# Kernel optimization log

Hardware: AMD Instinct MI355X
Metric: run time of the kernel (lower is better)

The kernel has to match this reference:

```python
import jax, jax.numpy as jnp
import numpy as np

B, S, D = 2, 2048, 4096
H, G, HD = 32, 8, 128          # num_heads, num_kv_groups, head_dim
GROUP = H // G                  # group_size = 4
SCALE = HD ** -0.5


def setup_inputs() -> dict:
    key = jax.random.key(0)
    ks = jax.random.split(key, 6)
    x = jax.random.normal(ks[0], (B, S, D), dtype=jnp.float32)
    # Linear weights stored as [in, out] (y = x @ W), no bias, 0.02 init scale
    Wq = jax.random.normal(ks[1], (D, H * HD), dtype=jnp.float32) * 0.02
    Wk = jax.random.normal(ks[2], (D, G * HD), dtype=jnp.float32) * 0.02
    Wv = jax.random.normal(ks[3], (D, G * HD), dtype=jnp.float32) * 0.02
    Wo = jax.random.normal(ks[4], (H * HD, D), dtype=jnp.float32) * 0.02
    # RoPE tables: [S, HD], duplicated-half layout (rotate-half convention)
    inv_freq = 1.0 / (10000.0 ** (jnp.arange(0, HD, 2, dtype=jnp.float32) / HD))
    angles = jnp.arange(S, dtype=jnp.float32)[:, None] * inv_freq[None, :]  # [S, HD/2]
    angles = jnp.concatenate([angles, angles], axis=-1)                      # [S, HD]
    cos = jnp.cos(angles)
    sin = jnp.sin(angles)
    # causal mask: True = masked (strict upper triangle)
    mask = jnp.triu(jnp.ones((S, S), dtype=bool), k=1)
    return {"x": x, "Wq": Wq, "Wk": Wk, "Wv": Wv, "Wo": Wo,
            "cos": cos, "sin": sin, "mask": mask, "start_pos": 0}


def _rope(t, cos, sin, offset):
    # t: [B, h, S, HD]; cos/sin: [S_total, HD]
    n = t.shape[2]
    c = jax.lax.dynamic_slice_in_dim(cos, offset, n, axis=0)  # [n, HD]
    s = jax.lax.dynamic_slice_in_dim(sin, offset, n, axis=0)
    t1, t2 = t[..., : HD // 2], t[..., HD // 2:]
    rotated = jnp.concatenate([-t2, t1], axis=-1)
    return t * c[None, None] + rotated * s[None, None]


def reference(x, Wq, Wk, Wv, Wo, cos, sin, mask, start_pos):
    # projections
    q = (x @ Wq).reshape(B, S, H, HD).transpose(0, 2, 1, 3)   # [B,H,S,HD]
    k = (x @ Wk).reshape(B, S, G, HD).transpose(0, 2, 1, 3)   # [B,G,S,HD]
    v = (x @ Wv).reshape(B, S, G, HD).transpose(0, 2, 1, 3)   # [B,G,S,HD]
    # RoPE (no cache: prev_len = 0)
    q = _rope(q, cos, sin, start_pos) * SCALE
    k = _rope(k, cos, sin, start_pos)
    # GQA: expand kv groups to full heads (repeat_interleave along head dim)
    k_r = jnp.repeat(k, GROUP, axis=1)                         # [B,H,S,HD]
    v_r = jnp.repeat(v, GROUP, axis=1)
    scores = jnp.einsum('bhqd,bhkd->bhqk', q, k_r)             # [B,H,S,S]
    scores = jnp.where(mask[None, None], -jnp.inf, scores)
    w = jax.nn.softmax(scores, axis=-1)
    ctx = jnp.einsum('bhqk,bhkd->bhqd', w, v_r)                # [B,H,S,HD]
    ctx = ctx.transpose(0, 2, 1, 3).reshape(B, S, H * HD)
    out = ctx @ Wo                                             # [B,S,D]
    return out
```

## Files before the change

### kernel.cpp

```cpp
#include <hip/hip_runtime.h>
#include <hip/hip_bf16.h>
#include <math.h>

#define B_ 2
#define S_ 2048
#define D_ 4096
#define H_ 32
#define G_ 8
#define HD_ 128
#define GROUP_ 4
#define SCALE_ 0.08838834764831845f

typedef short bfv8 __attribute__((ext_vector_type(8)));
typedef float f32x4 __attribute__((ext_vector_type(4)));

__device__ __forceinline__ f32x4 mfma16(bfv8 a, bfv8 b, f32x4 c) {
  return __builtin_amdgcn_mfma_f32_16x16x32_bf16(a, b, c, 0, 0, 0);
}

__device__ __forceinline__ ushort f2bf_bits(float f) {
  __hip_bfloat16 h = __float2bfloat16(f);
  return *reinterpret_cast<ushort*>(&h);
}

__device__ __forceinline__ void gload16(const short* g, short* l) {
  __builtin_amdgcn_global_load_lds(
      (const __attribute__((address_space(1))) void*)g,
      (__attribute__((address_space(3))) void*)l, 16, 0, 0);
}

__global__ __launch_bounds__(256) void k_cvt(const float* __restrict__ in,
                                             ushort* __restrict__ out, int n4) {
  int i = blockIdx.x * 256 + threadIdx.x;
  if (i >= n4) return;
  float4 v = *(const float4*)(in + (size_t)i * 4);
  ushort4 o;
  o.x = f2bf_bits(v.x); o.y = f2bf_bits(v.y); o.z = f2bf_bits(v.z); o.w = f2bf_bits(v.w);
  *(ushort4*)(out + (size_t)i * 4) = o;
}

__global__ __launch_bounds__(256) void k_transpose(const float* __restrict__ in,
                                                   ushort* __restrict__ out,
                                                   int R, int C) {
  __shared__ ushort tile[32][33];
  int bc = blockIdx.x * 32;
  int br = blockIdx.y * 32;
  int tx = threadIdx.x;
  int ty = threadIdx.y;
  for (int ii = 0; ii < 4; ii++) {
    int i = ty + ii * 8;
    tile[i][tx] = f2bf_bits(in[(size_t)(br + i) * C + bc + tx]);
  }
  __syncthreads();
  for (int ii = 0; ii < 4; ii++) {
    int i = ty + ii * 8;
    out[(size_t)(bc + i) * R + br + tx] = tile[tx][i];
  }
}

__global__ __launch_bounds__(256) void k_transpose_v(const ushort* __restrict__ v,
                                                     ushort* __restrict__ vt) {
  __shared__ ushort tile[32][33];
  int bg = blockIdx.z;
  int b = bg / G_, g = bg % G_;
  int s0 = blockIdx.y * 32;
  int h0 = blockIdx.x * 32;
  int tx = threadIdx.x, ty = threadIdx.y;
  const ushort* src = v + (size_t)b * S_ * G_ * HD_ + (size_t)g * HD_;
  ushort* dst = vt + (size_t)(b * G_ + g) * HD_ * S_;
  for (int ii = 0; ii < 4; ii++) {
    int i = ty + ii * 8;
    tile[i][tx] = src[(size_t)(s0 + i) * (G_ * HD_) + h0 + tx];
  }
  __syncthreads();
  for (int ii = 0; ii < 4; ii++) {
    int i = ty + ii * 8;
    dst[(size_t)(h0 + i) * S_ + s0 + tx] = tile[tx][i];
  }
}

__global__ __launch_bounds__(64) void k_rope(__hip_bfloat16* __restrict__ t,
                                             const float* __restrict__ cosb,
                                             const float* __restrict__ sinb,
                                             int nheads, float scale) {
  int blk = blockIdx.x;
  int head = blk % nheads;
  int row = blk / nheads;
  int s = row & (S_ - 1);
  int l = threadIdx.x;
  size_t base = (size_t)row * nheads * HD_ + (size_t)head * HD_;
  float x1 = __bfloat162float(t[base + l]);
  float x2 = __bfloat162float(t[base + 64 + l]);
  float c1 = cosb[s * HD_ + l];
  float sn1 = sinb[s * HD_ + l];
  float c2 = cosb[s * HD_ + 64 + l];
  float sn2 = sinb[s * HD_ + 64 + l];
  t[base + l] = __float2bfloat16((x1 * c1 - x2 * sn1) * scale);
  t[base + 64 + l] = __float2bfloat16((x2 * c2 + x1 * sn2) * scale);
}

template <typename OT>
__global__ __launch_bounds__(256) void k_gemm_bt(const __hip_bfloat16* __restrict__ Ab,
                                                 const __hip_bfloat16* __restrict__ BTb,
                                                 OT* __restrict__ Cb,
                                                 int M, int N, int K) {
  __shared__ short sA[128 * 32];
  __shared__ short sB[128 * 32];
  int t = threadIdx.x;
  int w = t >> 6;
  int l = t & 63;
  int row0 = blockIdx.y * 128;
  int col0 = blockIdx.x * 128;
  int wr = (w >> 1) * 64;
  int wc = (w & 1) * 64;
  int fr = l & 15;
  int fq = l >> 4;
  int fo = fq * 8;
  int srow = l >> 2;
  int schk = (l & 3) * 8;

  const short* gA = (const short*)Ab;
  const short* gB = (const short*)BTb;

  f32x4 acc[4][4];
#pragma unroll
  for (int m = 0; m < 4; m++)
#pragma unroll
    for (int n = 0; n < 4; n++) acc[m][n] = (f32x4){0.f, 0.f, 0.f, 0.f};

  for (int k0 = 0; k0 < K; k0 += 32) {
    __syncthreads();
#pragma unroll
    for (int j = 0; j < 2; j++) {
      int r = w * 32 + j * 16;
      gload16(gA + (size_t)(row0 + r + srow) * K + k0 + schk, &sA[r * 32]);
      gload16(gB + (size_t)(col0 + r + srow) * K + k0 + schk, &sB[r * 32]);
    }
    __syncthreads();
    bfv8 af[4], bff[4];
#pragma unroll
    for (int m = 0; m < 4; m++) af[m] = *(const bfv8*)(sA + (wr + m * 16 + fr) * 32 + fo);
#pragma unroll
    for (int n = 0; n < 4; n++) bff[n] = *(const bfv8*)(sB + (wc + n * 16 + fr) * 32 + fo);
#pragma unroll
    for (int m = 0; m < 4; m++)
#pragma unroll
      for (int n = 0; n < 4; n++)
        acc[m][n] = mfma16(af[m], bff[n], acc[m][n]);
  }
#pragma unroll
  for (int m = 0; m < 4; m++)
#pragma unroll
    for (int n = 0; n < 4; n++)
#pragma unroll
      for (int j = 0; j < 4; j++) {
        int r = row0 + wr + m * 16 + fq * 4 + j;
        int c = col0 + wc + n * 16 + fr;
        if constexpr (__is_same(OT, float)) {
          Cb[(size_t)r * N + c] = acc[m][n][j];
        } else {
          Cb[(size_t)r * N + c] = __float2bfloat16(acc[m][n][j]);
        }
      }
}

template <typename OT>
__global__ __launch_bounds__(512, 2) void k_gemm256(const __hip_bfloat16* __restrict__ Ab,
                                                    const __hip_bfloat16* __restrict__ BTb,
                                                    OT* __restrict__ Cb,
                                                    int M, int N, int K) {
  __shared__ short sA[2][2][8192];
  __shared__ short sB[2][2][8192];
  int tid = threadIdx.x;
  int wid = tid >> 6;
  int l = tid & 63;
  int wr = (wid >> 2) * 128;
  int wc = (wid & 3) * 64;
  int fr = l & 15, fq = l >> 4;
  int cswz = (fq ^ ((fr >> 1) & 3)) * 8;
  int row0 = blockIdx.y * 256, col0 = blockIdx.x * 256;
  int sr = l >> 2;
  int schunk = ((l & 3) ^ (((wid * 16 + sr) >> 1) & 3)) * 8;
  const short* gA = (const short*)Ab;
  const short* gB = (const short*)BTb;

  f32x4 acc[8][4];
#pragma unroll
  for (int m = 0; m < 8; m++)
#pragma unroll
    for (int n = 0; n < 4; n++) acc[m][n] = (f32x4){0.f, 0.f, 0.f, 0.f};

#define STAGE256(buf, kh, isB, kt)                                                   \
  {                                                                                  \
    const short* g_ = (isB) ? gB : gA;                                               \
    int b0_ = (isB) ? col0 : row0;                                                   \
    short* s_ = (isB) ? &sB[buf][kh][0] : &sA[buf][kh][0];                           \
    int k0_ = (kt) * 64 + (kh) * 32;                                                 \
    _Pragma("unroll")                                                                \
    for (int i_ = 0; i_ < 2; i_++) {                                                 \
      int r_ = i_ * 128 + wid * 16 + sr;                                             \
      gload16(g_ + (size_t)(b0_ + r_) * K + k0_ + schunk,                            \
              s_ + (i_ * 128 + wid * 16) * 32);                                      \
    }                                                                                \
  }

  bfv8 bf[4];
#define COMPUTE256(cur, kh, mg, loadB)                                               \
  {                                                                                  \
    if (loadB) {                                                                     \
      _Pragma("unroll")                                                              \
      for (int n_ = 0; n_ < 4; n_++)                                                 \
        bf[n_] = *(const bfv8*)&sB[cur][kh][(wc + n_ * 16 + fr) * 32 + cswz];        \
    }                                                                                \
    bfv8 af_[4];                                                                     \
    _Pragma("unroll")                                                                \
    for (int j_ = 0; j_ < 4; j_++)                                                   \
      af_[j_] = *(const bfv8*)&sA[cur][kh][(wr + ((mg) * 4 + j_) * 16 + fr) * 32 + cswz]; \
    __builtin_amdgcn_s_setprio(1);                                                   \
    _Pragma("unroll")                                                                \
    for (int j_ = 0; j_ < 4; j_++)                                                   \
      _Pragma("unroll")                                                              \
      for (int n_ = 0; n_ < 4; n_++)                                                 \
        acc[(mg) * 4 + j_][n_] = mfma16(af_[j_], bf[n_], acc[(mg) * 4 + j_][n_]);    \
    __builtin_amdgcn_s_setprio(0);                                                   \
  }

  int NT = K / 64;
  STAGE256(0, 0, false, 0);
  STAGE256(0, 0, true, 0);
  STAGE256(0, 1, false, 0);
  STAGE256(0, 1, true, 0);

  for (int t = 0; t < NT - 1; t++) {
    int cur = t & 1, nxt = cur ^ 1;
    asm volatile("s_waitcnt vmcnt(4)" ::: "memory");
    __builtin_amdgcn_s_barrier();
    STAGE256(nxt, 0, false, t + 1);
    COMPUTE256(cur, 0, 0, true);
    STAGE256(nxt, 0, true, t + 1);
    COMPUTE256(cur, 0, 1, false);
    asm volatile("s_waitcnt vmcnt(4)" ::: "memory");
    __builtin_amdgcn_s_barrier();
    STAGE256(nxt, 1, false, t + 1);
    COMPUTE256(cur, 1, 0, true);
    STAGE256(nxt, 1, true, t + 1);
    COMPUTE256(cur, 1, 1, false);
  }
  {
    int cur = (NT - 1) & 1;
    asm volatile("s_waitcnt vmcnt(4)" ::: "memory");
    __builtin_amdgcn_s_barrier();
    COMPUTE256(cur, 0, 0, true);
    COMPUTE256(cur, 0, 1, false);
    asm volatile("s_waitcnt vmcnt(0)" ::: "memory");
    __builtin_amdgcn_s_barrier();
    COMPUTE256(cur, 1, 0, true);
    COMPUTE256(cur, 1, 1, false);
  }
#undef STAGE256
#undef COMPUTE256

#pragma unroll
  for (int m = 0; m < 8; m++)
#pragma unroll
    for (int n = 0; n < 4; n++)
#pragma unroll
      for (int j = 0; j < 4; j++) {
        int r = row0 + wr + m * 16 + fq * 4 + j;
        int c = col0 + wc + n * 16 + fr;
        if constexpr (__is_same(OT, float)) {
          Cb[(size_t)r * N + c] = acc[m][n][j];
        } else {
          Cb[(size_t)r * N + c] = __float2bfloat16(acc[m][n][j]);
        }
      }
}

#define PSTR 68
__global__ __launch_bounds__(512) void k_attn2(const __hip_bfloat16* __restrict__ Qb,
                                               const __hip_bfloat16* __restrict__ Kb,
                                               const __hip_bfloat16* __restrict__ VTb,
                                               __hip_bfloat16* __restrict__ ctx) {
  __shared__ short sK[64 * 128];
  __shared__ short sV[128 * 64];
  __shared__ short sP[8][16 * PSTR];

  const int nQB = S_ / 128;
  int blk = blockIdx.x;
  int qb = (nQB - 1) - (blk % nQB);
  int bh = blk / nQB;
  int h = bh % H_;
  int b = bh / H_;
  int g = h / GROUP_;
  int q0 = qb * 128;

  int t = threadIdx.x;
  int wid = t >> 6;
  int l = t & 63;
  int fr = l & 15, fq = l >> 4, fo = fq * 8;
  int wq0 = q0 + wid * 16;

  const short* qp = (const short*)Qb + (size_t)b * S_ * H_ * HD_ + (size_t)h * HD_;
  const short* kp = (const short*)Kb + (size_t)b * S_ * G_ * HD_ + (size_t)g * HD_;
  const short* vp = (const short*)VTb + (size_t)(b * G_ + g) * HD_ * S_;

  bfv8 qf[4];
#pragma unroll
  for (int c = 0; c < 4; c++)
    qf[c] = *(const bfv8*)(qp + (size_t)(wq0 + fr) * (H_ * HD_) + c * 32 + fo);

  f32x4 acc[8];
#pragma unroll
  for (int n = 0; n < 8; n++) acc[n] = (f32x4){0.f, 0.f, 0.f, 0.f};
  float m[4], ll[4];
#pragma unroll
  for (int j = 0; j < 4; j++) { m[j] = -INFINITY; ll[j] = 0.f; }

  int krow_i = l >> 4;
  int kchk = l & 15;
  int vrow_i = l >> 3;
  int vchk = l & 7;

  int nkt = 2 * qb + 2;
  for (int kt = 0; kt < nkt; kt++) {
    int k0 = kt * 64;
#pragma unroll
    for (int j = 0; j < 2; j++) {
      int base = wid * 8 + j * 4;
      int r = base + krow_i;
      gload16(kp + (size_t)(k0 + r) * (G_ * HD_) + ((kchk ^ (r & 7)) * 8), &sK[base * 128]);
    }
#pragma unroll
    for (int j = 0; j < 2; j++) {
      int base = wid * 16 + j * 8;
      int r = base + vrow_i;
      gload16(vp + (size_t)r * S_ + k0 + ((vchk ^ (r & 7)) * 8), &sV[base * 64]);
    }
    __syncthreads();

    f32x4 sf[4];
#pragma unroll
    for (int ks = 0; ks < 4; ks++) {
      sf[ks] = (f32x4){0.f, 0.f, 0.f, 0.f};
      int row = ks * 16 + fr;
      int rx = row & 7;
#pragma unroll
      for (int c = 0; c < 4; c++) {
        bfv8 kf = *(const bfv8*)&sK[row * 128 + (((c * 4 + fq) ^ rx) * 8)];
        sf[ks] = mfma16(qf[c], kf, sf[ks]);
      }
    }

    float p[4][4], sc[4], red[4];
#pragma unroll
    for (int j = 0; j < 4; j++) {
      int q = wq0 + fq * 4 + j;
#pragma unroll
      for (int ks = 0; ks < 4; ks++)
        if (k0 + ks * 16 + fr > q) sf[ks][j] = -INFINITY;
      red[j] = fmaxf(fmaxf(sf[0][j], sf[1][j]), fmaxf(sf[2][j], sf[3][j]));
    }
#pragma unroll
    for (int off = 1; off < 16; off <<= 1)
#pragma unroll
      for (int j = 0; j < 4; j++)
        red[j] = fmaxf(red[j], __shfl_xor(red[j], off, 64));
#pragma unroll
    for (int j = 0; j < 4; j++) {
      float nm = fmaxf(m[j], red[j]);
      sc[j] = __expf(m[j] - nm);
      m[j] = nm;
#pragma unroll
      for (int ks = 0; ks < 4; ks++) p[ks][j] = __expf(sf[ks][j] - nm);
      red[j] = (p[0][j] + p[1][j]) + (p[2][j] + p[3][j]);
    }
#pragma unroll
    for (int off = 1; off < 16; off <<= 1)
#pragma unroll
      for (int j = 0; j < 4; j++)
        red[j] += __shfl_xor(red[j], off, 64);
#pragma unroll
    for (int j = 0; j < 4; j++) {
      ll[j] = ll[j] * sc[j] + red[j];
#pragma unroll
      for (int n = 0; n < 8; n++) acc[n][j] *= sc[j];
#pragma unroll
      for (int ks = 0; ks < 4; ks++)
        sP[wid][(fq * 4 + j) * PSTR + ks * 16 + fr] = f2bf_bits(p[ks][j]);
    }

    bfv8 pa0 = *(const bfv8*)&sP[wid][fr * PSTR + fo];
    bfv8 pa1 = *(const bfv8*)&sP[wid][fr * PSTR + 32 + fo];
#pragma unroll
    for (int n = 0; n < 8; n++) {
      int row = n * 16 + fr;
      int rx = row & 7;
      bfv8 vf0 = *(const bfv8*)&sV[row * 64 + ((fq ^ rx) * 8)];
      bfv8 vf1 = *(const bfv8*)&sV[row * 64 + (((4 + fq) ^ rx) * 8)];
      acc[n] = mfma16(pa0, vf0, acc[n]);
      acc[n] = mfma16(pa1, vf1, acc[n]);
    }
    __syncthreads();
  }

#pragma unroll
  for (int n = 0; n < 8; n++)
#pragma unroll
    for (int j = 0; j < 4; j++) {
      int q = wq0 + fq * 4 + j;
      float o = acc[n][j] / ll[j];
      ctx[(size_t)(b * S_ + q) * (H_ * HD_) + h * HD_ + n * 16 + fr] = __float2bfloat16(o);
    }
}

extern "C" void kernel_launch(void* const* d_in, const int* in_sizes, int n_in,
                              void* d_out, int out_size, void* d_ws, size_t ws_size,
                              hipStream_t stream) {
  (void)in_sizes; (void)n_in; (void)out_size; (void)ws_size;
  const float* x    = (const float*)d_in[0];
  const float* Wq   = (const float*)d_in[1];
  const float* Wk   = (const float*)d_in[2];
  const float* Wv   = (const float*)d_in[3];
  const float* Wo   = (const float*)d_in[4];
  const float* cosb = (const float*)d_in[5];
  const float* sinb = (const float*)d_in[6];

  char* ws = (char*)d_ws;
  __hip_bfloat16* xb  = (__hip_bfloat16*)(ws + 0);
  __hip_bfloat16* WqT = (__hip_bfloat16*)(ws + 33554432);
  __hip_bfloat16* WkT = (__hip_bfloat16*)(ws + 67108864);
  __hip_bfloat16* WvT = (__hip_bfloat16*)(ws + 75497472);
  __hip_bfloat16* Qb  = (__hip_bfloat16*)(ws + 83886080);
  __hip_bfloat16* Kb  = (__hip_bfloat16*)(ws + 117440512);
  __hip_bfloat16* Vb  = (__hip_bfloat16*)(ws + 125829120);
  __hip_bfloat16* VTb = (__hip_bfloat16*)(ws + 134217728);
  __hip_bfloat16* Cx  = xb;

  dim3 tb(32, 8);
  k_cvt<<<(B_ * S_ * D_ / 4 + 255) / 256, 256, 0, stream>>>(x, (ushort*)xb, B_ * S_ * D_ / 4);
  k_transpose<<<dim3(128, 128), tb, 0, stream>>>(Wq, (ushort*)WqT, 4096, 4096);
  k_transpose<<<dim3(32, 128), tb, 0, stream>>>(Wk, (ushort*)WkT, 4096, 1024);
  k_transpose<<<dim3(32, 128), tb, 0, stream>>>(Wv, (ushort*)WvT, 4096, 1024);

  k_gemm256<__hip_bfloat16><<<dim3(16, 16), 512, 0, stream>>>(xb, WqT, Qb, 4096, 4096, 4096);
  k_gemm_bt<__hip_bfloat16><<<dim3(8, 32), 256, 0, stream>>>(xb, WkT, Kb, 4096, 1024, 4096);
  k_gemm_bt<__hip_bfloat16><<<dim3(8, 32), 256, 0, stream>>>(xb, WvT, Vb, 4096, 1024, 4096);

  k_transpose<<<dim3(128, 128), tb, 0, stream>>>(Wo, (ushort*)WqT, 4096, 4096);

  k_rope<<<4096 * 32, 64, 0, stream>>>(Qb, cosb, sinb, 32, SCALE_);
  k_rope<<<4096 * 8, 64, 0, stream>>>(Kb, cosb, sinb, 8, 1.0f);

  k_transpose_v<<<dim3(4, 64, 16), tb, 0, stream>>>((const ushort*)Vb, (ushort*)VTb);

  k_attn2<<<B_ * H_ * (S_ / 128), 512, 0, stream>>>(Qb, Kb, VTb, Cx);

  k_gemm256<float><<<dim3(16, 16), 512, 0, stream>>>(Cx, WqT, (float*)d_out, 4096, 4096, 4096);
}
```

Measured before the change: 829.5 us.

## Fuse K/V projection GEMMs, vectorize weight transpose, batch RoPE heads per block

Merges the K and V projections into one GEMM by treating the adjacent WkT/WvT buffers as a single 2048-wide weight, writing an interleaved KV buffer that attention and the V transpose read with a doubled stride. The fp32-to-bf16 weight transpose now uses float4 loads and ushort4 stores with a 1D block. RoPE processes four heads per 256-thread block instead of one head per 64-thread block. These aim to cut launch count and improve memory efficiency in the small pre-processing kernels, at the cost of relying on the workspace adjacency of the K and V weights.

```diff
diff --git a/kernel.cpp b/kernel.cpp
--- a/kernel.cpp
+++ b/kernel.cpp
@@ -9,6 +9,7 @@
 #define G_ 8
 #define HD_ 128
 #define GROUP_ 4
+#define KVSTR_ (2 * G_ * HD_)
 #define SCALE_ 0.08838834764831845f
 
 typedef short bfv8 __attribute__((ext_vector_type(8)));
@@ -42,35 +43,42 @@
 __global__ __launch_bounds__(256) void k_transpose(const float* __restrict__ in,
                                                    ushort* __restrict__ out,
                                                    int R, int C) {
-  __shared__ ushort tile[32][33];
+  __shared__ ushort tile[32][36];
   int bc = blockIdx.x * 32;
   int br = blockIdx.y * 32;
-  int tx = threadIdx.x;
-  int ty = threadIdx.y;
-  for (int ii = 0; ii < 4; ii++) {
-    int i = ty + ii * 8;
-    tile[i][tx] = f2bf_bits(in[(size_t)(br + i) * C + bc + tx]);
-  }
+  int t = threadIdx.x;
+  int rr = t >> 3;
+  int c4 = (t & 7) * 4;
+  float4 v = *(const float4*)(in + (size_t)(br + rr) * C + bc + c4);
+  tile[rr][c4 + 0] = f2bf_bits(v.x);
+  tile[rr][c4 + 1] = f2bf_bits(v.y);
+  tile[rr][c4 + 2] = f2bf_bits(v.z);
+  tile[rr][c4 + 3] = f2bf_bits(v.w);
   __syncthreads();
-  for (int ii = 0; ii < 4; ii++) {
-    int i = ty + ii * 8;
-    out[(size_t)(bc + i) * R + br + tx] = tile[tx][i];
-  }
+  int cc = t >> 3;
+  int r4 = (t & 7) * 4;
+  ushort4 o;
+  o.x = tile[r4 + 0][cc];
+  o.y = tile[r4 + 1][cc];
+  o.z = tile[r4 + 2][cc];
+  o.w = tile[r4 + 3][cc];
+  *(ushort4*)(out + (size_t)(bc + cc) * R + br + r4) = o;
 }
 
 __global__ __launch_bounds__(256) void k_transpose_v(const ushort* __restrict__ v,
-                                                     ushort* __restrict__ vt) {
+                                                     ushort* __restrict__ vt,
+                                                     int hstride, int hoff) {
   __shared__ ushort tile[32][33];
   int bg = blockIdx.z;
   int b = bg / G_, g = bg % G_;
   int s0 = blockIdx.y * 32;
   int h0 = blockIdx.x * 32;
   int tx = threadIdx.x, ty = threadIdx.y;
-  const ushort* src = v + (size_t)b * S_ * G_ * HD_ + (size_t)g * HD_;
+  const ushort* src = v + (size_t)b * S_ * hstride + (size_t)(hoff + g) * HD_;
   ushort* dst = vt + (size_t)(b * G_ + g) * HD_ * S_;
   for (int ii = 0; ii < 4; ii++) {
     int i = ty + ii * 8;
-    tile[i][tx] = src[(size_t)(s0 + i) * (G_ * HD_) + h0 + tx];
+    tile[i][tx] = src[(size_t)(s0 + i) * hstride + h0 + tx];
   }
   __syncthreads();
   for (int ii = 0; ii < 4; ii++) {
@@ -79,16 +87,16 @@
   }
 }
 
-__global__ __launch_bounds__(64) void k_rope(__hip_bfloat16* __restrict__ t,
-                                             const float* __restrict__ cosb,
-                                             const float* __restrict__ sinb,
-                                             int nheads, float scale) {
-  int blk = blockIdx.x;
-  int head = blk % nheads;
-  int row = blk / nheads;
+__global__ __launch_bounds__(256) void k_rope(__hip_bfloat16* __restrict__ t,
+                                              const float* __restrict__ cosb,
+                                              const float* __restrict__ sinb,
+                                              int hstride, int nlaunch, float scale) {
+  int item = blockIdx.x * 4 + (threadIdx.x >> 6);
+  int head = item % nlaunch;
+  int row = item / nlaunch;
   int s = row & (S_ - 1);
-  int l = threadIdx.x;
-  size_t base = (size_t)row * nheads * HD_ + (size_t)head * HD_;
+  int l = threadIdx.x & 63;
+  size_t base = (size_t)row * hstride * HD_ + (size_t)head * HD_;
   float x1 = __bfloat162float(t[base + l]);
   float x2 = __bfloat162float(t[base + 64 + l]);
   float c1 = cosb[s * HD_ + l];
@@ -278,7 +286,7 @@
 
 #define PSTR 68
 __global__ __launch_bounds__(512) void k_attn2(const __hip_bfloat16* __restrict__ Qb,
-                                               const __hip_bfloat16* __restrict__ Kb,
+                                               const __hip_bfloat16* __restrict__ KVb,
                                                const __hip_bfloat16* __restrict__ VTb,
                                                __hip_bfloat16* __restrict__ ctx) {
   __shared__ short sK[64 * 128];
@@ -301,7 +309,7 @@
   int wq0 = q0 + wid * 16;
 
   const short* qp = (const short*)Qb + (size_t)b * S_ * H_ * HD_ + (size_t)h * HD_;
-  const short* kp = (const short*)Kb + (size_t)b * S_ * G_ * HD_ + (size_t)g * HD_;
+  const short* kp = (const short*)KVb + (size_t)b * S_ * KVSTR_ + (size_t)g * HD_;
   const short* vp = (const short*)VTb + (size_t)(b * G_ + g) * HD_ * S_;
 
   bfv8 qf[4];
@@ -328,7 +336,7 @@
     for (int j = 0; j < 2; j++) {
       int base = wid * 8 + j * 4;
       int r = base + krow_i;
-      gload16(kp + (size_t)(k0 + r) * (G_ * HD_) + ((kchk ^ (r & 7)) * 8), &sK[base * 128]);
+      gload16(kp + (size_t)(k0 + r) * KVSTR_ + ((kchk ^ (r & 7)) * 8), &sK[base * 128]);
     }
 #pragma unroll
     for (int j = 0; j < 2; j++) {
@@ -431,29 +439,27 @@
   __hip_bfloat16* WkT = (__hip_bfloat16*)(ws + 67108864);
   __hip_bfloat16* WvT = (__hip_bfloat16*)(ws + 75497472);
   __hip_bfloat16* Qb  = (__hip_bfloat16*)(ws + 83886080);
-  __hip_bfloat16* Kb  = (__hip_bfloat16*)(ws + 117440512);
-  __hip_bfloat16* Vb  = (__hip_bfloat16*)(ws + 125829120);
+  __hip_bfloat16* KVb = (__hip_bfloat16*)(ws + 117440512);
   __hip_bfloat16* VTb = (__hip_bfloat16*)(ws + 134217728);
   __hip_bfloat16* Cx  = xb;
 
-  dim3 tb(32, 8);
   k_cvt<<<(B_ * S_ * D_ / 4 + 255) / 256, 256, 0, stream>>>(x, (ushort*)xb, B_ * S_ * D_ / 4);
-  k_transpose<<<dim3(128, 128), tb, 0, stream>>>(Wq, (ushort*)WqT, 4096, 4096);
-  k_transpose<<<dim3(32, 128), tb, 0, stream>>>(Wk, (ushort*)WkT, 4096, 1024);
-  k_transpose<<<dim3(32, 128), tb, 0, stream>>>(Wv, (ushort*)WvT, 4096, 1024);
+  k_transpose<<<dim3(128, 128), 256, 0, stream>>>(Wq, (ushort*)WqT, 4096, 4096);
+  k_transpose<<<dim3(32, 128), 256, 0, stream>>>(Wk, (ushort*)WkT, 4096, 1024);
+  k_transpose<<<dim3(32, 128), 256, 0, stream>>>(Wv, (ushort*)WvT, 4096, 1024);
 
   k_gemm256<__hip_bfloat16><<<dim3(16, 16), 512, 0, stream>>>(xb, WqT, Qb, 4096, 4096, 4096);
-  k_gemm_bt<__hip_bfloat16><<<dim3(8, 32), 256, 0, stream>>>(xb, WkT, Kb, 4096, 1024, 4096);
-  k_gemm_bt<__hip_bfloat16><<<dim3(8, 32), 256, 0, stream>>>(xb, WvT, Vb, 4096, 1024, 4096);
-
-  k_transpose<<<dim3(128, 128), tb, 0, stream>>>(Wo, (ushort*)WqT, 4096, 4096);
-
-  k_rope<<<4096 * 32, 64, 0, stream>>>(Qb, cosb, sinb, 32, SCALE_);
-  k_rope<<<4096 * 8, 64, 0, stream>>>(Kb, cosb, sinb, 8, 1.0f);
-
-  k_transpose_v<<<dim3(4, 64, 16), tb, 0, stream>>>((const ushort*)Vb, (ushort*)VTb);
-
-  k_attn2<<<B_ * H_ * (S_ / 128), 512, 0, stream>>>(Qb, Kb, VTb, Cx);
+  k_gemm_bt<__hip_bfloat16><<<dim3(16, 32), 256, 0, stream>>>(xb, WkT, KVb, 4096, 2048, 4096);
+
+  k_transpose<<<dim3(128, 128), 256, 0, stream>>>(Wo, (ushort*)WqT, 4096, 4096);
+
+  k_rope<<<4096 * 32 / 4, 256, 0, stream>>>(Qb, cosb, sinb, 32, 32, SCALE_);
+  k_rope<<<4096 * 8 / 4, 256, 0, stream>>>((__hip_bfloat16*)KVb, cosb, sinb, 16, 8, 1.0f);
+
+  k_transpose_v<<<dim3(4, 64, 16), dim3(32, 8), 0, stream>>>((const ushort*)KVb, (ushort*)VTb,
+                                                             KVSTR_, G_);
+
+  k_attn2<<<B_ * H_ * (S_ / 128), 512, 0, stream>>>(Qb, KVb, VTb, Cx);
 
   k_gemm256<float><<<dim3(16, 16), 512, 0, stream>>>(Cx, WqT, (float*)d_out, 4096, 4096, 4096);
 }
```

Measured after the change: 737.9 us. -11.0%, faster.
